# Optimization experiments

Measured on AMD Instinct MI355X. Metric: run time of the kernel, lower is better.

Reference implementation:

```python
import jax, jax.numpy as jnp
import numpy as np

B, TM1, K, H = 256, 127, 128, 256  # batch, time_step-1, input_size, hidden

def setup_inputs() -> dict:
    key = jax.random.key(0)
    ks = jax.random.split(key, 7)
    s_ih = 1.0 / np.sqrt(H)
    return {
        "input_data": jax.random.normal(ks[0], (B, TM1, K), dtype=jnp.float32),
        "W_ih": jax.random.uniform(ks[1], (4 * H, K), jnp.float32, -s_ih, s_ih),
        "W_hh": jax.random.uniform(ks[2], (4 * H, H), jnp.float32, -s_ih, s_ih),
        "b_ih": jax.random.uniform(ks[3], (4 * H,), jnp.float32, -s_ih, s_ih),
        "b_hh": jax.random.uniform(ks[4], (4 * H,), jnp.float32, -s_ih, s_ih),
        "fc_w": jax.random.uniform(ks[5], (1, 2 * H + TM1), jnp.float32, -s_ih, s_ih),
        "fc_b": jax.random.uniform(ks[6], (1,), jnp.float32, -s_ih, s_ih),
    }

def reference(input_data, W_ih, W_hh, b_ih, b_hh, fc_w, fc_b):
    b, tm1, k = input_data.shape
    h_dim = W_hh.shape[1]
    w = fc_w[0]
    W_h, W_c, W_x = w[:h_dim], w[h_dim:2 * h_dim], w[2 * h_dim:]
    # attention score contribution from each series' full history: constant over steps
    x_score = jnp.einsum('btk,t->bk', input_data, W_x) + fc_b[0]  # (B, K)
    bias = b_ih + b_hh

    def step(carry, xt):
        h, c = carry  # (B, H) each; xt: (B, K) values at current timestep
        scores = x_score + (h @ W_h + c @ W_c)[:, None]  # (B, K)
        alpha = jax.nn.softmax(scores, axis=-1)
        x = alpha * xt  # attention-weighted input
        gates = x @ W_ih.T + h @ W_hh.T + bias  # (B, 4H), torch gate order i,f,g,o
        i, f, g, o = jnp.split(gates, 4, axis=-1)
        c_new = jax.nn.sigmoid(f) * c + jax.nn.sigmoid(i) * jnp.tanh(g)
        h_new = jax.nn.sigmoid(o) * jnp.tanh(c_new)
        return (h_new, c_new), (x, h_new)

    h0 = jnp.zeros((b, h_dim), input_data.dtype)
    c0 = jnp.zeros((b, h_dim), input_data.dtype)
    xt_seq = jnp.swapaxes(input_data, 0, 1)  # (TM1, B, K)
    _, (xs, hs) = jax.lax.scan(step, (h0, c0), xt_seq)
    weight = jnp.swapaxes(xs, 0, 1)        # (B, TM1, K)
    encode_weight = jnp.swapaxes(hs, 0, 1)  # (B, TM1, H)
    return weight, encode_weight
```

## Files before the change

kernel.cpp:

```cpp
#include <hip/hip_runtime.h>
#include <hip/hip_bf16.h>
#include <stdint.h>

#define Bn 256
#define Tn 127
#define Kn 128
#define Hn 256

typedef float f32x4 __attribute__((ext_vector_type(4)));
typedef short s16x8 __attribute__((ext_vector_type(8)));

#define GX_BYTES   66584576ULL
#define REC_OFF    66584576ULL
#define REC_BYTES  1048576ULL

__device__ __forceinline__ float bf2f(unsigned short b){
  union { unsigned u; float f; } v; v.u = ((unsigned)b) << 16; return v.f;
}
__device__ __forceinline__ unsigned short f2bf_rn(float f){
  union { __hip_bfloat16 h; unsigned short s; } u;
  u.h = __float2bfloat16(f);
  return u.s;
}
__device__ __forceinline__ s16x8 cvt8(f32x4 a, f32x4 b){
  union { __hip_bfloat162 h2; unsigned short s[2]; } u0,u1,u2,u3;
  u0.h2 = __float22bfloat162_rn(float2{a[0],a[1]});
  u1.h2 = __float22bfloat162_rn(float2{a[2],a[3]});
  u2.h2 = __float22bfloat162_rn(float2{b[0],b[1]});
  u3.h2 = __float22bfloat162_rn(float2{b[2],b[3]});
  s16x8 r;
  r[0]=(short)u0.s[0]; r[1]=(short)u0.s[1]; r[2]=(short)u1.s[0]; r[3]=(short)u1.s[1];
  r[4]=(short)u2.s[0]; r[5]=(short)u2.s[1]; r[6]=(short)u3.s[0]; r[7]=(short)u3.s[1];
  return r;
}
__device__ __forceinline__ float sigf(float x){ return 1.f/(1.f+__expf(-x)); }
__device__ __forceinline__ float tanh_fast(float x){
  float ax = fabsf(x);
  float e = __expf(-2.f*ax);
  float t = (1.f - e)/(1.f + e);
  return x < 0.f ? -t : t;
}

__global__ __launch_bounds__(256) void phase0_kernel(
    const float* __restrict__ in, const float* __restrict__ fc_w,
    float* __restrict__ out)
{
  const int b    = blockIdx.x;
  const int tid  = threadIdx.x;
  const int k    = tid & 127;
  const int half = tid >> 7;
  __shared__ float wx[Tn+1];
  __shared__ float partial[2][128];
  __shared__ float red[8];
  __shared__ float alpha_s[128];
  if (tid < Tn) wx[tid] = fc_w[2*Hn + tid];
  __syncthreads();

  const float* ib = in + (size_t)b*Tn*Kn;
  const int t0 = half*64, t1 = half ? Tn : 64;
  float acc = 0.f;
  for (int t=t0; t<t1; t++) acc += ib[t*Kn + k] * wx[t];
  partial[half][k] = acc;
  __syncthreads();
  const float tot = partial[0][k] + partial[1][k];

  float mx = tot;
#pragma unroll
  for (int o=32;o>0;o>>=1) mx = fmaxf(mx, __shfl_xor(mx, o));
  const int wv = tid >> 6;
  if ((tid & 63) == 0) red[wv] = mx;
  __syncthreads();
  mx = fmaxf(fmaxf(red[0],red[1]), fmaxf(red[2],red[3]));
  float e = __expf(tot - mx);
  float sm = e;
#pragma unroll
  for (int o=32;o>0;o>>=1) sm += __shfl_xor(sm, o);
  if ((tid & 63) == 0) red[4+wv] = sm;
  __syncthreads();
  if (half == 0) alpha_s[k] = e / (red[4] + red[5]);
  __syncthreads();

  const int k4 = tid & 31;
  const int tr = tid >> 5;
  const f32x4 al4 = *(const f32x4*)&alpha_s[k4*4];
  float* ob = out + (size_t)b*Tn*Kn;
  for (int t=tr; t<Tn; t+=8){
    f32x4 v = *(const f32x4*)(ib + t*Kn + k4*4);
    v[0]*=al4[0]; v[1]*=al4[1]; v[2]*=al4[2]; v[3]*=al4[3];
    *(f32x4*)(ob + t*Kn + k4*4) = v;
  }
}

__global__ __launch_bounds__(256) void gx_kernel(
    const float* __restrict__ xw, const float* __restrict__ W_ih,
    const float* __restrict__ b_ih, const float* __restrict__ b_hh,
    __hip_bfloat16* __restrict__ gx)
{
  const int g    = blockIdx.x & 31;
  const int tpb  = blockIdx.x >> 5;
  const int tid  = threadIdx.x;
  const int wv   = tid >> 6;
  const int lane = tid & 63;
  const int c    = lane & 15;
  const int quad = lane >> 4;

  const int b  = g*8 + (c & 7);

  s16x8 afr[4][4];
#pragma unroll
  for (int tpi=0; tpi<4; tpi++){
    const int t0 = (tpb*4 + tpi)*2;
    const int tt = min(t0 + (c >> 3), Tn-1);
    const float* xp = xw + ((size_t)b*Tn + tt)*Kn + quad*8;
#pragma unroll
    for (int kb=0; kb<4; kb++)
      afr[tpi][kb] = cvt8(*(const f32x4*)(xp + kb*32), *(const f32x4*)(xp + kb*32 + 4));
  }

  const int tof = (quad >> 1);
  const int mh  = (quad & 1) * 4;

  for (int j = wv*16; j < wv*16+16; j++){
    const int n = j*16 + c;
    const float bias = b_ih[n] + b_hh[n];
    const float* wp = W_ih + (size_t)n*Kn + quad*8;
    s16x8 bfr[4];
#pragma unroll
    for (int kb=0; kb<4; kb++)
      bfr[kb] = cvt8(*(const f32x4*)(wp + kb*32), *(const f32x4*)(wp + kb*32 + 4));
    const int G = j >> 4, rem = j & 15, s = rem >> 3, w8 = rem & 7;
#pragma unroll
    for (int tpi=0; tpi<4; tpi++){
      f32x4 acc = {bias, bias, bias, bias};
#pragma unroll
      for (int kb=0; kb<4; kb++)
        acc = __builtin_amdgcn_mfma_f32_16x16x32_bf16(afr[tpi][kb], bfr[kb], acc, 0,0,0);
      const int trow = (tpb*4 + tpi)*2 + tof;
      if (trow < Tn){
        __hip_bfloat16* dst = gx +
          (((((size_t)g*Tn + trow)*2 + s)*8 + w8)*4 + G)*128 + c*8 + mh;
        ushort4 pk;
        pk.x = f2bf_rn(acc[0]); pk.y = f2bf_rn(acc[1]);
        pk.z = f2bf_rn(acc[2]); pk.w = f2bf_rn(acc[3]);
        *(ushort4*)dst = pk;
      }
    }
  }
}

__global__ __launch_bounds__(512, 2) void scan_kernel(
    const float* __restrict__ W_hh, float* __restrict__ out,
    const __hip_bfloat16* __restrict__ gx,
    unsigned long long* __restrict__ rec)
{
  const int bid  = blockIdx.x;
  const int s    = (bid >> 3) & 1;
  const int g    = (bid & 7) | ((bid >> 4) << 3);
  const int b0   = g * 8;
  const int tid  = threadIdx.x;
  const int w    = tid >> 6;
  const int lane = tid & 63;
  const int c    = lane & 15;
  const int quad = lane >> 4;
  const int u    = s*128 + w*16 + c;

  __shared__ __align__(16) unsigned short hhi[2*8*272];
  __shared__ __align__(16) unsigned short hlo[2*8*272];

  s16x8 whh[4][8];
#pragma unroll
  for (int G=0; G<4; G++){
    const float* p0 = W_hh + (size_t)(G*Hn + u)*Hn + quad*8;
#pragma unroll
    for (int kb=0; kb<8; kb++)
      whh[G][kb] = cvt8(*(const f32x4*)(p0 + kb*32), *(const f32x4*)(p0 + kb*32 + 4));
  }

  const int rsel0 = (quad >> 1) * 2;
  const int prr0  = rsel0 ^ 2;
  const int m0    = (quad & 1)*4 + rsel0;
  float cst[2] = {0.f, 0.f};

  const size_t enc_base = (size_t)Bn*Tn*Kn;
  unsigned long long* rec_mine  = rec + ((size_t)g*2 + s)*2048;
  unsigned long long* rec_other = rec + ((size_t)g*2 + (1-s))*2048;

  const int rq   = lane >> 4;
  const int r_m0 = (rq & 1)*4 + (rq >> 1)*2;
  const int r_u  = w*16 + c;
  const int rk   = (1-s)*128 + r_u;

  const __hip_bfloat16* gxg = gx + ((((size_t)g*Tn)*2 + s)*8 + w)*4*128;

  ushort4 gxr[4];
  if (quad < 2){
    const __hip_bfloat16* gp0 = gxg + c*8 + quad*4;
#pragma unroll
    for (int G=0; G<4; G++) gxr[G] = *(const ushort4*)(gp0 + G*128);
  }

  for (int t=0; t<Tn; t++){
    const int buf  = (t & 1) * 8*272;
    const int nbuf = ((t+1) & 1) * 8*272;

    f32x4 acc[4];
#pragma unroll
    for (int G=0; G<4; G++){
      if (quad < 2){
        acc[G][0]=bf2f(gxr[G].x); acc[G][1]=bf2f(gxr[G].y);
        acc[G][2]=bf2f(gxr[G].z); acc[G][3]=bf2f(gxr[G].w);
      } else {
        acc[G][0]=0.f; acc[G][1]=0.f; acc[G][2]=0.f; acc[G][3]=0.f;
      }
    }

    if (t > 0){
      const unsigned short* hb = (c < 8) ? &hhi[buf + c*272] : &hlo[buf + (c-8)*272];
#pragma unroll
      for (int kb=0; kb<8; kb++){
        const s16x8 af = *(const s16x8*)(hb + kb*32 + quad*8);
        acc[0] = __builtin_amdgcn_mfma_f32_16x16x32_bf16(af, whh[0][kb], acc[0],0,0,0);
        acc[1] = __builtin_amdgcn_mfma_f32_16x16x32_bf16(af, whh[1][kb], acc[1],0,0,0);
        acc[2] = __builtin_amdgcn_mfma_f32_16x16x32_bf16(af, whh[2][kb], acc[2],0,0,0);
        acc[3] = __builtin_amdgcn_mfma_f32_16x16x32_bf16(af, whh[3][kb], acc[3],0,0,0);
      }
    }

    float hv[2];
#pragma unroll
    for (int rp=0; rp<2; rp++){
      const int rr  = rsel0 + rp;
      const int prr = prr0 + rp;
      const float gi = acc[0][rr] + __shfl_xor(acc[0][prr], 32);
      const float gf = acc[1][rr] + __shfl_xor(acc[1][prr], 32);
      const float gg = acc[2][rr] + __shfl_xor(acc[2][prr], 32);
      const float go = acc[3][rr] + __shfl_xor(acc[3][prr], 32);
      const float cn = sigf(gf)*cst[rp] + sigf(gi)*tanh_fast(gg);
      cst[rp] = cn;
      hv[rp] = sigf(go)*tanh_fast(cn);
    }

    unsigned short hi[2], lo[2];
    hi[0] = f2bf_rn(hv[0]); lo[0] = f2bf_rn(hv[0] - bf2f(hi[0]));
    hi[1] = f2bf_rn(hv[1]); lo[1] = f2bf_rn(hv[1] - bf2f(hi[1]));
    if (t < Tn-1){
      const unsigned tg16 = ((unsigned)(t+1)) << 16;
      const unsigned long long w0 =
          (unsigned long long)((unsigned)hi[0] | tg16) |
          ((unsigned long long)((unsigned)hi[1] | tg16) << 32);
      const unsigned long long w1 =
          (unsigned long long)((unsigned)lo[0] | tg16) |
          ((unsigned long long)((unsigned)lo[1] | tg16) << 32);
      unsigned long long* rm = rec_mine + (size_t)(t & 1)*1024 + 2*tid;
      __hip_atomic_store(rm,   w0, __ATOMIC_RELAXED, __HIP_MEMORY_SCOPE_AGENT);
      __hip_atomic_store(rm+1, w1, __ATOMIC_RELAXED, __HIP_MEMORY_SCOPE_AGENT);
    }

#pragma unroll
    for (int rp=0; rp<2; rp++){
      const int m = m0 + rp;
      hhi[nbuf + m*272 + u] = hi[rp];
      hlo[nbuf + m*272 + u] = lo[rp];
      out[enc_base + ((size_t)(b0+m)*Tn + t)*Hn + u] = hv[rp];
    }

    if (t+1 < Tn && quad < 2){
      const __hip_bfloat16* gp = gxg + (size_t)(t+1)*2*8*4*128 + c*8 + quad*4;
#pragma unroll
      for (int G=0; G<4; G++) gxr[G] = *(const ushort4*)(gp + G*128);
    }

    if (t < Tn-1){
      const unsigned long long tg = (unsigned long long)(t+1);
      const unsigned long long* ro = rec_other + (size_t)(t & 1)*1024 + 2*tid;
      unsigned long long w0, w1;
      for (;;){
        w0 = __hip_atomic_load(ro,   __ATOMIC_RELAXED, __HIP_MEMORY_SCOPE_AGENT);
        w1 = __hip_atomic_load(ro+1, __ATOMIC_RELAXED, __HIP_MEMORY_SCOPE_AGENT);
        if ( ((w0 >> 16) & 0xffffu) == tg && (w0 >> 48) == tg &&
             ((w1 >> 16) & 0xffffu) == tg && (w1 >> 48) == tg ) break;
        __builtin_amdgcn_s_sleep(1);
      }
      hhi[nbuf + r_m0*272 + rk]     = (unsigned short)(w0 & 0xffffu);
      hlo[nbuf + r_m0*272 + rk]     = (unsigned short)(w1 & 0xffffu);
      hhi[nbuf + (r_m0+1)*272 + rk] = (unsigned short)((w0 >> 32) & 0xffffu);
      hlo[nbuf + (r_m0+1)*272 + rk] = (unsigned short)((w1 >> 32) & 0xffffu);
    }

    __syncthreads();
  }
}

extern "C" void kernel_launch(void* const* d_in, const int* in_sizes, int n_in,
                              void* d_out, int out_size, void* d_ws, size_t ws_size,
                              hipStream_t stream) {
  const float* input = (const float*)d_in[0];
  const float* W_ih  = (const float*)d_in[1];
  const float* W_hh  = (const float*)d_in[2];
  const float* b_ih  = (const float*)d_in[3];
  const float* b_hh  = (const float*)d_in[4];
  const float* fc_w  = (const float*)d_in[5];
  float* out = (float*)d_out;

  char* wsb = (char*)d_ws;
  __hip_bfloat16* gxp = (__hip_bfloat16*)wsb;
  unsigned long long* rec = (unsigned long long*)(wsb + REC_OFF);

  hipMemsetAsync(rec, 0, REC_BYTES, stream);
  phase0_kernel<<<Bn, 256, 0, stream>>>(input, fc_w, out);
  gx_kernel<<<512, 256, 0, stream>>>(out, W_ih, b_ih, b_hh, gxp);
  scan_kernel<<<64, 512, 0, stream>>>(W_hh, out, gxp, rec);
}
```

Before: 474.7 us.

## Add L2-local fast path for cross-block hidden-state exchange with fallback

The scan kernel's per-step exchange of hidden-state halves between paired blocks gets a second record buffer. Each step writes a 128-bit store through the plain path and also does the existing agent-scope atomic stores. The consumer polls with sc0 128-bit loads for a bounded number of spins before falling back to the old atomic polling loop. This aims to cut the latency of the inter-block handshake on the serial critical path. The fast path assumes both blocks see the same L2, which may not hold on MI355X's multi-XCD layout, so it relies on the miss counter to switch itself off, and it adds extra stores every step.

```diff
diff --git a/kernel.cpp b/kernel.cpp
--- a/kernel.cpp
+++ b/kernel.cpp
@@ -9,10 +9,12 @@
 
 typedef float f32x4 __attribute__((ext_vector_type(4)));
 typedef short s16x8 __attribute__((ext_vector_type(8)));
-
-#define GX_BYTES   66584576ULL
-#define REC_OFF    66584576ULL
-#define REC_BYTES  1048576ULL
+typedef unsigned int u32x4 __attribute__((ext_vector_type(4)));
+
+#define GX_BYTES    66584576ULL
+#define RECL2_OFF   66584576ULL
+#define REC_BYTES   1048576ULL
+#define RECIC_OFF   (RECL2_OFF + REC_BYTES)
 
 __device__ __forceinline__ float bf2f(unsigned short b){
   union { unsigned u; float f; } v; v.u = ((unsigned)b) << 16; return v.f;
@@ -39,6 +41,16 @@
   float e = __expf(-2.f*ax);
   float t = (1.f - e)/(1.f + e);
   return x < 0.f ? -t : t;
+}
+
+__device__ __forceinline__ u32x4 ld_b128_sc0(const void* p){
+  u32x4 r;
+  asm volatile("global_load_dwordx4 %0, %1, off sc0\n\ts_waitcnt vmcnt(0)"
+               : "=v"(r) : "v"(p) : "memory");
+  return r;
+}
+__device__ __forceinline__ void st_b128_l2(void* p, u32x4 v){
+  asm volatile("global_store_dwordx4 %0, %1, off" :: "v"(p), "v"(v) : "memory");
 }
 
 __global__ __launch_bounds__(256) void phase0_kernel(
@@ -151,7 +163,7 @@
 __global__ __launch_bounds__(512, 2) void scan_kernel(
     const float* __restrict__ W_hh, float* __restrict__ out,
     const __hip_bfloat16* __restrict__ gx,
-    unsigned long long* __restrict__ rec)
+    unsigned long long* __restrict__ recL2, unsigned long long* __restrict__ recIC)
 {
   const int bid  = blockIdx.x;
   const int s    = (bid >> 3) & 1;
@@ -182,8 +194,10 @@
   float cst[2] = {0.f, 0.f};
 
   const size_t enc_base = (size_t)Bn*Tn*Kn;
-  unsigned long long* rec_mine  = rec + ((size_t)g*2 + s)*2048;
-  unsigned long long* rec_other = rec + ((size_t)g*2 + (1-s))*2048;
+  unsigned long long* recL2_mine  = recL2 + ((size_t)g*2 + s)*2048;
+  unsigned long long* recL2_other = recL2 + ((size_t)g*2 + (1-s))*2048;
+  unsigned long long* recIC_mine  = recIC + ((size_t)g*2 + s)*2048;
+  unsigned long long* recIC_other = recIC + ((size_t)g*2 + (1-s))*2048;
 
   const int rq   = lane >> 4;
   const int r_m0 = (rq & 1)*4 + (rq >> 1)*2;
@@ -198,6 +212,9 @@
 #pragma unroll
     for (int G=0; G<4; G++) gxr[G] = *(const ushort4*)(gp0 + G*128);
   }
+
+  bool fastok = true;
+  int  misses = 0;
 
   for (int t=0; t<Tn; t++){
     const int buf  = (t & 1) * 8*272;
@@ -245,15 +262,17 @@
     hi[1] = f2bf_rn(hv[1]); lo[1] = f2bf_rn(hv[1] - bf2f(hi[1]));
     if (t < Tn-1){
       const unsigned tg16 = ((unsigned)(t+1)) << 16;
+      u32x4 r;
+      r[0] = (unsigned)hi[0] | tg16; r[1] = (unsigned)hi[1] | tg16;
+      r[2] = (unsigned)lo[0] | tg16; r[3] = (unsigned)lo[1] | tg16;
+      st_b128_l2(recL2_mine + (size_t)(t & 1)*1024 + 2*tid, r);
       const unsigned long long w0 =
-          (unsigned long long)((unsigned)hi[0] | tg16) |
-          ((unsigned long long)((unsigned)hi[1] | tg16) << 32);
+          (unsigned long long)r[0] | ((unsigned long long)r[1] << 32);
       const unsigned long long w1 =
-          (unsigned long long)((unsigned)lo[0] | tg16) |
-          ((unsigned long long)((unsigned)lo[1] | tg16) << 32);
-      unsigned long long* rm = rec_mine + (size_t)(t & 1)*1024 + 2*tid;
-      __hip_atomic_store(rm,   w0, __ATOMIC_RELAXED, __HIP_MEMORY_SCOPE_AGENT);
-      __hip_atomic_store(rm+1, w1, __ATOMIC_RELAXED, __HIP_MEMORY_SCOPE_AGENT);
+          (unsigned long long)r[2] | ((unsigned long long)r[3] << 32);
+      unsigned long long* rmIC = recIC_mine + (size_t)(t & 1)*1024 + 2*tid;
+      __hip_atomic_store(rmIC,   w0, __ATOMIC_RELAXED, __HIP_MEMORY_SCOPE_AGENT);
+      __hip_atomic_store(rmIC+1, w1, __ATOMIC_RELAXED, __HIP_MEMORY_SCOPE_AGENT);
     }
 
 #pragma unroll
@@ -271,20 +290,43 @@
     }
 
     if (t < Tn-1){
-      const unsigned long long tg = (unsigned long long)(t+1);
-      const unsigned long long* ro = rec_other + (size_t)(t & 1)*1024 + 2*tid;
-      unsigned long long w0, w1;
-      for (;;){
-        w0 = __hip_atomic_load(ro,   __ATOMIC_RELAXED, __HIP_MEMORY_SCOPE_AGENT);
-        w1 = __hip_atomic_load(ro+1, __ATOMIC_RELAXED, __HIP_MEMORY_SCOPE_AGENT);
-        if ( ((w0 >> 16) & 0xffffu) == tg && (w0 >> 48) == tg &&
-             ((w1 >> 16) & 0xffffu) == tg && (w1 >> 48) == tg ) break;
-        __builtin_amdgcn_s_sleep(1);
-      }
-      hhi[nbuf + r_m0*272 + rk]     = (unsigned short)(w0 & 0xffffu);
-      hlo[nbuf + r_m0*272 + rk]     = (unsigned short)(w1 & 0xffffu);
-      hhi[nbuf + (r_m0+1)*272 + rk] = (unsigned short)((w0 >> 32) & 0xffffu);
-      hlo[nbuf + (r_m0+1)*272 + rk] = (unsigned short)((w1 >> 32) & 0xffffu);
+      const unsigned tg = (unsigned)(t+1);
+      const unsigned long long* roL2 = recL2_other + (size_t)(t & 1)*1024 + 2*tid;
+      const unsigned long long* roIC = recIC_other + (size_t)(t & 1)*1024 + 2*tid;
+      unsigned short vh0, vh1, vl0, vl1;
+      bool got = false;
+      if (fastok){
+        const int nspin = (t == 0) ? 4000 : 64;
+        for (int sp=0; sp<nspin; ++sp){
+          u32x4 r = ld_b128_sc0(roL2);
+          if ((r[0]>>16)==tg && (r[1]>>16)==tg && (r[2]>>16)==tg && (r[3]>>16)==tg){
+            vh0=(unsigned short)r[0]; vh1=(unsigned short)r[1];
+            vl0=(unsigned short)r[2]; vl1=(unsigned short)r[3];
+            got = true; break;
+          }
+        }
+        if (!got){ if (++misses >= 2) fastok = false; }
+        else misses = 0;
+      }
+      if (!got){
+        for (;;){
+          const unsigned long long w0 =
+            __hip_atomic_load(roIC,   __ATOMIC_RELAXED, __HIP_MEMORY_SCOPE_AGENT);
+          const unsigned long long w1 =
+            __hip_atomic_load(roIC+1, __ATOMIC_RELAXED, __HIP_MEMORY_SCOPE_AGENT);
+          if (((w0 >> 16) & 0xffffu) == tg && (w0 >> 48) == tg &&
+              ((w1 >> 16) & 0xffffu) == tg && (w1 >> 48) == tg){
+            vh0=(unsigned short)w0; vh1=(unsigned short)(w0 >> 32);
+            vl0=(unsigned short)w1; vl1=(unsigned short)(w1 >> 32);
+            break;
+          }
+          __builtin_amdgcn_s_sleep(1);
+        }
+      }
+      hhi[nbuf + r_m0*272 + rk]     = vh0;
+      hhi[nbuf + (r_m0+1)*272 + rk] = vh1;
+      hlo[nbuf + r_m0*272 + rk]     = vl0;
+      hlo[nbuf + (r_m0+1)*272 + rk] = vl1;
     }
 
     __syncthreads();
@@ -304,10 +346,12 @@
 
   char* wsb = (char*)d_ws;
   __hip_bfloat16* gxp = (__hip_bfloat16*)wsb;
-  unsigned long long* rec = (unsigned long long*)(wsb + REC_OFF);
-
-  hipMemsetAsync(rec, 0, REC_BYTES, stream);
+  unsigned long long* recL2 = (unsigned long long*)(wsb + RECL2_OFF);
+  const bool dual = (ws_size >= RECIC_OFF + REC_BYTES);
+  unsigned long long* recIC = dual ? (unsigned long long*)(wsb + RECIC_OFF) : recL2;
+
+  hipMemsetAsync(recL2, 0, dual ? 2*REC_BYTES : REC_BYTES, stream);
   phase0_kernel<<<Bn, 256, 0, stream>>>(input, fc_w, out);
   gx_kernel<<<512, 256, 0, stream>>>(out, W_ih, b_ih, b_hh, gxp);
-  scan_kernel<<<64, 512, 0, stream>>>(W_hh, out, gxp, rec);
-}
+  scan_kernel<<<64, 512, 0, stream>>>(W_hh, out, gxp, recL2, recIC);
+}
```

After: 1.496 ms. 3.15x slower.

## Split recurrent matmul over K across block pairs with partial-sum exchange

Applied to the files above, without the earlier changes.

Adds a scan variant in which the two blocks serving a batch group each own half of the hidden input dimension. Each block computes its own partial gate sums plus the partial sums for the other block's units, and swaps those through tagged 64-bit atomic stores in global memory with spin-wait polling, instead of exchanging full hidden states. The weights are converted to bf16 once by a new kernel, so the gx and scan kernels load them directly instead of converting per thread. The new path only runs when the workspace is large enough. Packing a step tag into the low mantissa bits drops some precision from the partial sums, and the per-step cross-block handshake now sits on the critical path.

```diff
diff --git a/kernel.cpp b/kernel.cpp
--- a/kernel.cpp
+++ b/kernel.cpp
@@ -11,8 +11,12 @@
 typedef short s16x8 __attribute__((ext_vector_type(8)));
 
 #define GX_BYTES   66584576ULL
-#define REC_OFF    66584576ULL
+#define PART_OFF   66584576ULL
+#define PART_BYTES 2097152ULL
 #define REC_BYTES  1048576ULL
+#define WIH_OFF    (PART_OFF + PART_BYTES)
+#define WHH_OFF    (WIH_OFF + 262144ULL)
+#define WS_NEED    (WHH_OFF + 524288ULL)
 
 __device__ __forceinline__ float bf2f(unsigned short b){
   union { unsigned u; float f; } v; v.u = ((unsigned)b) << 16; return v.f;
@@ -39,6 +43,20 @@
   float e = __expf(-2.f*ax);
   float t = (1.f - e)/(1.f + e);
   return x < 0.f ? -t : t;
+}
+
+__global__ __launch_bounds__(256) void wconv_kernel(
+    const float* __restrict__ Wih, const float* __restrict__ Whh,
+    __hip_bfloat16* __restrict__ Bih, __hip_bfloat16* __restrict__ Bhh)
+{
+  const int i = blockIdx.x*256 + threadIdx.x;
+  const float* src; __hip_bfloat16* dst; int j;
+  if (i < 16384){ src = Wih; dst = Bih; j = i; }
+  else          { src = Whh; dst = Bhh; j = i - 16384; }
+  const f32x4 a = *(const f32x4*)(src + (size_t)j*8);
+  const f32x4 b = *(const f32x4*)(src + (size_t)j*8 + 4);
+  s16x8 r = cvt8(a, b);
+  *(s16x8*)(dst + (size_t)j*8) = r;
 }
 
 __global__ __launch_bounds__(256) void phase0_kernel(
@@ -93,8 +111,9 @@
 
 __global__ __launch_bounds__(256) void gx_kernel(
     const float* __restrict__ xw, const float* __restrict__ W_ih,
+    const __hip_bfloat16* __restrict__ Bih,
     const float* __restrict__ b_ih, const float* __restrict__ b_hh,
-    __hip_bfloat16* __restrict__ gx)
+    __hip_bfloat16* __restrict__ gx, int pre)
 {
   const int g    = blockIdx.x & 31;
   const int tpb  = blockIdx.x >> 5;
@@ -123,11 +142,17 @@
   for (int j = wv*16; j < wv*16+16; j++){
     const int n = j*16 + c;
     const float bias = b_ih[n] + b_hh[n];
-    const float* wp = W_ih + (size_t)n*Kn + quad*8;
     s16x8 bfr[4];
-#pragma unroll
-    for (int kb=0; kb<4; kb++)
-      bfr[kb] = cvt8(*(const f32x4*)(wp + kb*32), *(const f32x4*)(wp + kb*32 + 4));
+    if (pre){
+      const __hip_bfloat16* wp = Bih + (size_t)n*Kn + quad*8;
+#pragma unroll
+      for (int kb=0; kb<4; kb++) bfr[kb] = *(const s16x8*)(wp + kb*32);
+    } else {
+      const float* wp = W_ih + (size_t)n*Kn + quad*8;
+#pragma unroll
+      for (int kb=0; kb<4; kb++)
+        bfr[kb] = cvt8(*(const f32x4*)(wp + kb*32), *(const f32x4*)(wp + kb*32 + 4));
+    }
     const int G = j >> 4, rem = j & 15, s = rem >> 3, w8 = rem & 7;
 #pragma unroll
     for (int tpi=0; tpi<4; tpi++){
@@ -148,7 +173,175 @@
   }
 }
 
-__global__ __launch_bounds__(512, 2) void scan_kernel(
+__global__ __launch_bounds__(512, 2) void scan_ksplit(
+    const __hip_bfloat16* __restrict__ Bhh,
+    float* __restrict__ out, const __hip_bfloat16* __restrict__ gx,
+    unsigned long long* __restrict__ part)
+{
+  const int bid  = blockIdx.x;
+  const int s    = (bid >> 3) & 1;
+  const int g    = (bid & 7) | ((bid >> 4) << 3);
+  const int b0   = g * 8;
+  const int tid  = threadIdx.x;
+  const int w    = tid >> 6;
+  const int lane = tid & 63;
+  const int c    = lane & 15;
+  const int quad = lane >> 4;
+  const int ul   = w*16 + c;
+  const int u    = s*128 + ul;
+
+  __shared__ __align__(16) unsigned short hhi[2*8*136];
+  __shared__ __align__(16) unsigned short hlo[2*8*136];
+
+  s16x8 whO[4][4], whT[4][4];
+#pragma unroll
+  for (int G=0; G<4; G++){
+    const __hip_bfloat16* pO = Bhh + ((size_t)(G*256 + s*128     + ul))*256 + s*128 + quad*8;
+    const __hip_bfloat16* pT = Bhh + ((size_t)(G*256 + (1-s)*128 + ul))*256 + s*128 + quad*8;
+#pragma unroll
+    for (int kb=0; kb<4; kb++){
+      whO[G][kb] = *(const s16x8*)(pO + kb*32);
+      whT[G][kb] = *(const s16x8*)(pT + kb*32);
+    }
+  }
+
+  const int rsel0 = (quad >> 1) * 2;
+  const int prr0  = rsel0 ^ 2;
+  const int m0    = (quad & 1)*4 + rsel0;
+  float cst[2] = {0.f, 0.f};
+
+  const size_t enc_base = (size_t)Bn*Tn*Kn;
+  unsigned long long* pmine  = part + (((size_t)g*2 + s)*2)*2048 + (size_t)tid*4;
+  unsigned long long* pother = part + (((size_t)g*2 + (1-s))*2)*2048 + (size_t)tid*4;
+
+  const __hip_bfloat16* gxg = gx + ((((size_t)g*Tn)*2 + s)*8 + w)*4*128;
+
+  ushort4 gxr[4];
+  if (quad < 2){
+    const __hip_bfloat16* gp0 = gxg + c*8 + quad*4;
+#pragma unroll
+    for (int G=0; G<4; G++) gxr[G] = *(const ushort4*)(gp0 + G*128);
+  }
+
+  for (int t=0; t<Tn; t++){
+    const int buf  = (t & 1) * 8*136;
+    const int nbuf = ((t+1) & 1) * 8*136;
+
+    f32x4 accO[4];
+#pragma unroll
+    for (int G=0; G<4; G++){
+      if (quad < 2){
+        accO[G][0]=bf2f(gxr[G].x); accO[G][1]=bf2f(gxr[G].y);
+        accO[G][2]=bf2f(gxr[G].z); accO[G][3]=bf2f(gxr[G].w);
+      } else {
+        accO[G][0]=0.f; accO[G][1]=0.f; accO[G][2]=0.f; accO[G][3]=0.f;
+      }
+    }
+
+    if (t > 0){
+      const unsigned short* hb = (c < 8) ? &hhi[buf + c*136] : &hlo[buf + (c-8)*136];
+      s16x8 af[4];
+#pragma unroll
+      for (int kb=0; kb<4; kb++)
+        af[kb] = *(const s16x8*)(hb + kb*32 + quad*8);
+
+      f32x4 accT[4];
+#pragma unroll
+      for (int G=0; G<4; G++){ accT[G][0]=0.f; accT[G][1]=0.f; accT[G][2]=0.f; accT[G][3]=0.f; }
+#pragma unroll
+      for (int kb=0; kb<4; kb++){
+        accT[0] = __builtin_amdgcn_mfma_f32_16x16x32_bf16(af[kb], whT[0][kb], accT[0],0,0,0);
+        accT[1] = __builtin_amdgcn_mfma_f32_16x16x32_bf16(af[kb], whT[1][kb], accT[1],0,0,0);
+        accT[2] = __builtin_amdgcn_mfma_f32_16x16x32_bf16(af[kb], whT[2][kb], accT[2],0,0,0);
+        accT[3] = __builtin_amdgcn_mfma_f32_16x16x32_bf16(af[kb], whT[3][kb], accT[3],0,0,0);
+      }
+
+      const unsigned tg = (unsigned)t & 0x7Fu;
+      unsigned long long* pm = pmine + (size_t)(t & 1)*2048;
+#pragma unroll
+      for (int G=0; G<4; G++){
+        const float p0 = accT[G][rsel0]   + __shfl_xor(accT[G][prr0],   32);
+        const float p1 = accT[G][rsel0+1] + __shfl_xor(accT[G][prr0+1], 32);
+        const unsigned d0 = (__float_as_uint(p0) & 0xFFFFFF80u) | tg;
+        const unsigned d1 = (__float_as_uint(p1) & 0xFFFFFF80u) | tg;
+        const unsigned long long q =
+            (unsigned long long)d0 | ((unsigned long long)d1 << 32);
+        __hip_atomic_store(pm + G, q, __ATOMIC_RELAXED, __HIP_MEMORY_SCOPE_AGENT);
+      }
+
+#pragma unroll
+      for (int kb=0; kb<4; kb++){
+        accO[0] = __builtin_amdgcn_mfma_f32_16x16x32_bf16(af[kb], whO[0][kb], accO[0],0,0,0);
+        accO[1] = __builtin_amdgcn_mfma_f32_16x16x32_bf16(af[kb], whO[1][kb], accO[1],0,0,0);
+        accO[2] = __builtin_amdgcn_mfma_f32_16x16x32_bf16(af[kb], whO[2][kb], accO[2],0,0,0);
+        accO[3] = __builtin_amdgcn_mfma_f32_16x16x32_bf16(af[kb], whO[3][kb], accO[3],0,0,0);
+      }
+    }
+
+    if (t+1 < Tn && quad < 2){
+      const __hip_bfloat16* gp = gxg + (size_t)(t+1)*2*8*4*128 + c*8 + quad*4;
+#pragma unroll
+      for (int G=0; G<4; G++) gxr[G] = *(const ushort4*)(gp + G*128);
+    }
+
+    float rv[4][2];
+    if (t > 0){
+      const unsigned tg = (unsigned)t & 0x7Fu;
+      const unsigned long long* po = pother + (size_t)(t & 1)*2048;
+      unsigned long long q0,q1,q2,q3;
+      for (;;){
+        q0 = __hip_atomic_load(po+0, __ATOMIC_RELAXED, __HIP_MEMORY_SCOPE_AGENT);
+        q1 = __hip_atomic_load(po+1, __ATOMIC_RELAXED, __HIP_MEMORY_SCOPE_AGENT);
+        q2 = __hip_atomic_load(po+2, __ATOMIC_RELAXED, __HIP_MEMORY_SCOPE_AGENT);
+        q3 = __hip_atomic_load(po+3, __ATOMIC_RELAXED, __HIP_MEMORY_SCOPE_AGENT);
+        if ( ((unsigned)q0 & 0x7Fu)==tg && ((unsigned)(q0>>32) & 0x7Fu)==tg &&
+             ((unsigned)q1 & 0x7Fu)==tg && ((unsigned)(q1>>32) & 0x7Fu)==tg &&
+             ((unsigned)q2 & 0x7Fu)==tg && ((unsigned)(q2>>32) & 0x7Fu)==tg &&
+             ((unsigned)q3 & 0x7Fu)==tg && ((unsigned)(q3>>32) & 0x7Fu)==tg ) break;
+        __builtin_amdgcn_s_sleep(1);
+      }
+      rv[0][0] = __uint_as_float((unsigned)q0 & 0xFFFFFF80u);
+      rv[0][1] = __uint_as_float((unsigned)(q0>>32) & 0xFFFFFF80u);
+      rv[1][0] = __uint_as_float((unsigned)q1 & 0xFFFFFF80u);
+      rv[1][1] = __uint_as_float((unsigned)(q1>>32) & 0xFFFFFF80u);
+      rv[2][0] = __uint_as_float((unsigned)q2 & 0xFFFFFF80u);
+      rv[2][1] = __uint_as_float((unsigned)(q2>>32) & 0xFFFFFF80u);
+      rv[3][0] = __uint_as_float((unsigned)q3 & 0xFFFFFF80u);
+      rv[3][1] = __uint_as_float((unsigned)(q3>>32) & 0xFFFFFF80u);
+    } else {
+#pragma unroll
+      for (int G=0; G<4; G++){ rv[G][0]=0.f; rv[G][1]=0.f; }
+    }
+
+    float hv[2];
+#pragma unroll
+    for (int rp=0; rp<2; rp++){
+      const int rr  = rsel0 + rp;
+      const int prr = prr0 + rp;
+      const float gi = accO[0][rr] + __shfl_xor(accO[0][prr], 32) + rv[0][rp];
+      const float gf = accO[1][rr] + __shfl_xor(accO[1][prr], 32) + rv[1][rp];
+      const float gg = accO[2][rr] + __shfl_xor(accO[2][prr], 32) + rv[2][rp];
+      const float go = accO[3][rr] + __shfl_xor(accO[3][prr], 32) + rv[3][rp];
+      const float cn = sigf(gf)*cst[rp] + sigf(gi)*tanh_fast(gg);
+      cst[rp] = cn;
+      hv[rp] = sigf(go)*tanh_fast(cn);
+    }
+
+#pragma unroll
+    for (int rp=0; rp<2; rp++){
+      const unsigned short hi = f2bf_rn(hv[rp]);
+      const unsigned short lo = f2bf_rn(hv[rp] - bf2f(hi));
+      const int m = m0 + rp;
+      hhi[nbuf + m*136 + ul] = hi;
+      hlo[nbuf + m*136 + ul] = lo;
+      out[enc_base + ((size_t)(b0+m)*Tn + t)*Hn + u] = hv[rp];
+    }
+
+    __syncthreads();
+  }
+}
+
+__global__ __launch_bounds__(512, 2) void scan_nsplit(
     const float* __restrict__ W_hh, float* __restrict__ out,
     const __hip_bfloat16* __restrict__ gx,
     unsigned long long* __restrict__ rec)
@@ -304,10 +497,23 @@
 
   char* wsb = (char*)d_ws;
   __hip_bfloat16* gxp = (__hip_bfloat16*)wsb;
-  unsigned long long* rec = (unsigned long long*)(wsb + REC_OFF);
-
-  hipMemsetAsync(rec, 0, REC_BYTES, stream);
-  phase0_kernel<<<Bn, 256, 0, stream>>>(input, fc_w, out);
-  gx_kernel<<<512, 256, 0, stream>>>(out, W_ih, b_ih, b_hh, gxp);
-  scan_kernel<<<64, 512, 0, stream>>>(W_hh, out, gxp, rec);
-}
+  unsigned long long* part = (unsigned long long*)(wsb + PART_OFF);
+
+  const int full = (ws_size >= WS_NEED) ? 1 : 0;
+
+  if (full){
+    __hip_bfloat16* Bih = (__hip_bfloat16*)(wsb + WIH_OFF);
+    __hip_bfloat16* Bhh = (__hip_bfloat16*)(wsb + WHH_OFF);
+    hipMemsetAsync(part, 0, PART_BYTES, stream);
+    wconv_kernel<<<192, 256, 0, stream>>>(W_ih, W_hh, Bih, Bhh);
+    phase0_kernel<<<Bn, 256, 0, stream>>>(input, fc_w, out);
+    gx_kernel<<<512, 256, 0, stream>>>(out, W_ih, Bih, b_ih, b_hh, gxp, 1);
+    scan_ksplit<<<64, 512, 0, stream>>>(Bhh, out, gxp, part);
+  } else {
+    hipMemsetAsync(part, 0, REC_BYTES, stream);
+    phase0_kernel<<<Bn, 256, 0, stream>>>(input, fc_w, out);
+    gx_kernel<<<512, 256, 0, stream>>>(out, W_ih, (const __hip_bfloat16*)W_ih,
+                                       b_ih, b_hh, gxp, 0);
+    scan_nsplit<<<64, 512, 0, stream>>>(W_hh, out, gxp, part);
+  }
+}
```

After: 604.9 us. 27.4% more time.

## Overlap peer h-state wait with own-half MFMA; pre-convert weights to bf16

Applied to the files above, without the earlier changes.

The scan loop now runs the MFMAs for its own half of the hidden state before polling for the partner block's half. It then fills that half into the current buffer, synchronises, and finishes the remaining MFMAs, so the cross-block wait overlaps with compute. The spin loop also drops its sleep. A separate kernel pre-converts W_ih and W_hh to bf16 in the workspace so gx_kernel and scan_kernel load bf16 directly instead of converting fp32 in each block. This adds an extra __syncthreads per step and a small extra launch, and the busy-wait without sleep may increase memory polling pressure.

```diff
diff --git a/kernel.cpp b/kernel.cpp
--- a/kernel.cpp
+++ b/kernel.cpp
@@ -13,6 +13,9 @@
 #define GX_BYTES   66584576ULL
 #define REC_OFF    66584576ULL
 #define REC_BYTES  1048576ULL
+#define WIH_OFF    (REC_OFF + REC_BYTES)
+#define WHH_OFF    (WIH_OFF + 262144ULL)
+#define WS_NEED    (WHH_OFF + 524288ULL)
 
 __device__ __forceinline__ float bf2f(unsigned short b){
   union { unsigned u; float f; } v; v.u = ((unsigned)b) << 16; return v.f;
@@ -39,6 +42,20 @@
   float e = __expf(-2.f*ax);
   float t = (1.f - e)/(1.f + e);
   return x < 0.f ? -t : t;
+}
+
+__global__ __launch_bounds__(256) void wconv_kernel(
+    const float* __restrict__ Wih, const float* __restrict__ Whh,
+    __hip_bfloat16* __restrict__ Bih, __hip_bfloat16* __restrict__ Bhh)
+{
+  const int i = blockIdx.x*256 + threadIdx.x;
+  const float* src; __hip_bfloat16* dst; int j;
+  if (i < 16384){ src = Wih; dst = Bih; j = i; }
+  else          { src = Whh; dst = Bhh; j = i - 16384; }
+  const f32x4 a = *(const f32x4*)(src + (size_t)j*8);
+  const f32x4 b = *(const f32x4*)(src + (size_t)j*8 + 4);
+  s16x8 r = cvt8(a, b);
+  *(s16x8*)(dst + (size_t)j*8) = r;
 }
 
 __global__ __launch_bounds__(256) void phase0_kernel(
@@ -93,8 +110,9 @@
 
 __global__ __launch_bounds__(256) void gx_kernel(
     const float* __restrict__ xw, const float* __restrict__ W_ih,
+    const __hip_bfloat16* __restrict__ Bih,
     const float* __restrict__ b_ih, const float* __restrict__ b_hh,
-    __hip_bfloat16* __restrict__ gx)
+    __hip_bfloat16* __restrict__ gx, int pre)
 {
   const int g    = blockIdx.x & 31;
   const int tpb  = blockIdx.x >> 5;
@@ -123,11 +141,17 @@
   for (int j = wv*16; j < wv*16+16; j++){
     const int n = j*16 + c;
     const float bias = b_ih[n] + b_hh[n];
-    const float* wp = W_ih + (size_t)n*Kn + quad*8;
     s16x8 bfr[4];
-#pragma unroll
-    for (int kb=0; kb<4; kb++)
-      bfr[kb] = cvt8(*(const f32x4*)(wp + kb*32), *(const f32x4*)(wp + kb*32 + 4));
+    if (pre){
+      const __hip_bfloat16* wp = Bih + (size_t)n*Kn + quad*8;
+#pragma unroll
+      for (int kb=0; kb<4; kb++) bfr[kb] = *(const s16x8*)(wp + kb*32);
+    } else {
+      const float* wp = W_ih + (size_t)n*Kn + quad*8;
+#pragma unroll
+      for (int kb=0; kb<4; kb++)
+        bfr[kb] = cvt8(*(const f32x4*)(wp + kb*32), *(const f32x4*)(wp + kb*32 + 4));
+    }
     const int G = j >> 4, rem = j & 15, s = rem >> 3, w8 = rem & 7;
 #pragma unroll
     for (int tpi=0; tpi<4; tpi++){
@@ -149,9 +173,9 @@
 }
 
 __global__ __launch_bounds__(512, 2) void scan_kernel(
-    const float* __restrict__ W_hh, float* __restrict__ out,
-    const __hip_bfloat16* __restrict__ gx,
-    unsigned long long* __restrict__ rec)
+    const float* __restrict__ W_hh, const __hip_bfloat16* __restrict__ Bhh,
+    float* __restrict__ out, const __hip_bfloat16* __restrict__ gx,
+    unsigned long long* __restrict__ rec, int pre)
 {
   const int bid  = blockIdx.x;
   const int s    = (bid >> 3) & 1;
@@ -168,13 +192,25 @@
   __shared__ __align__(16) unsigned short hlo[2*8*272];
 
   s16x8 whh[4][8];
-#pragma unroll
-  for (int G=0; G<4; G++){
-    const float* p0 = W_hh + (size_t)(G*Hn + u)*Hn + quad*8;
-#pragma unroll
-    for (int kb=0; kb<8; kb++)
-      whh[G][kb] = cvt8(*(const f32x4*)(p0 + kb*32), *(const f32x4*)(p0 + kb*32 + 4));
-  }
+  if (pre){
+#pragma unroll
+    for (int G=0; G<4; G++){
+      const __hip_bfloat16* p0 = Bhh + (size_t)(G*Hn + u)*Hn + quad*8;
+#pragma unroll
+      for (int kb=0; kb<8; kb++) whh[G][kb] = *(const s16x8*)(p0 + kb*32);
+    }
+  } else {
+#pragma unroll
+    for (int G=0; G<4; G++){
+      const float* p0 = W_hh + (size_t)(G*Hn + u)*Hn + quad*8;
+#pragma unroll
+      for (int kb=0; kb<8; kb++)
+        whh[G][kb] = cvt8(*(const f32x4*)(p0 + kb*32), *(const f32x4*)(p0 + kb*32 + 4));
+    }
+  }
+
+  const int kO = s*4;
+  const int kT = (1-s)*4;
 
   const int rsel0 = (quad >> 1) * 2;
   const int prr0  = rsel0 ^ 2;
@@ -216,8 +252,37 @@
 
     if (t > 0){
       const unsigned short* hb = (c < 8) ? &hhi[buf + c*272] : &hlo[buf + (c-8)*272];
-#pragma unroll
-      for (int kb=0; kb<8; kb++){
+
+#pragma unroll
+      for (int k4i=0; k4i<4; k4i++){
+        const int kb = kO + k4i;
+        const s16x8 af = *(const s16x8*)(hb + kb*32 + quad*8);
+        acc[0] = __builtin_amdgcn_mfma_f32_16x16x32_bf16(af, whh[0][kb], acc[0],0,0,0);
+        acc[1] = __builtin_amdgcn_mfma_f32_16x16x32_bf16(af, whh[1][kb], acc[1],0,0,0);
+        acc[2] = __builtin_amdgcn_mfma_f32_16x16x32_bf16(af, whh[2][kb], acc[2],0,0,0);
+        acc[3] = __builtin_amdgcn_mfma_f32_16x16x32_bf16(af, whh[3][kb], acc[3],0,0,0);
+      }
+
+      {
+        const unsigned long long tg = (unsigned long long)t;
+        const unsigned long long* ro = rec_other + (size_t)((t-1) & 1)*1024 + 2*tid;
+        unsigned long long w0, w1;
+        for (;;){
+          w0 = __hip_atomic_load(ro,   __ATOMIC_RELAXED, __HIP_MEMORY_SCOPE_AGENT);
+          w1 = __hip_atomic_load(ro+1, __ATOMIC_RELAXED, __HIP_MEMORY_SCOPE_AGENT);
+          if ( ((w0 >> 16) & 0xffffu) == tg && (w0 >> 48) == tg &&
+               ((w1 >> 16) & 0xffffu) == tg && (w1 >> 48) == tg ) break;
+        }
+        hhi[buf + r_m0*272 + rk]     = (unsigned short)(w0 & 0xffffu);
+        hlo[buf + r_m0*272 + rk]     = (unsigned short)(w1 & 0xffffu);
+        hhi[buf + (r_m0+1)*272 + rk] = (unsigned short)((w0 >> 32) & 0xffffu);
+        hlo[buf + (r_m0+1)*272 + rk] = (unsigned short)((w1 >> 32) & 0xffffu);
+      }
+      __syncthreads();
+
+#pragma unroll
+      for (int k4i=0; k4i<4; k4i++){
+        const int kb = kT + k4i;
         const s16x8 af = *(const s16x8*)(hb + kb*32 + quad*8);
         acc[0] = __builtin_amdgcn_mfma_f32_16x16x32_bf16(af, whh[0][kb], acc[0],0,0,0);
         acc[1] = __builtin_amdgcn_mfma_f32_16x16x32_bf16(af, whh[1][kb], acc[1],0,0,0);
@@ -270,23 +335,6 @@
       for (int G=0; G<4; G++) gxr[G] = *(const ushort4*)(gp + G*128);
     }
 
-    if (t < Tn-1){
-      const unsigned long long tg = (unsigned long long)(t+1);
-      const unsigned long long* ro = rec_other + (size_t)(t & 1)*1024 + 2*tid;
-      unsigned long long w0, w1;
-      for (;;){
-        w0 = __hip_atomic_load(ro,   __ATOMIC_RELAXED, __HIP_MEMORY_SCOPE_AGENT);
-        w1 = __hip_atomic_load(ro+1, __ATOMIC_RELAXED, __HIP_MEMORY_SCOPE_AGENT);
-        if ( ((w0 >> 16) & 0xffffu) == tg && (w0 >> 48) == tg &&
-             ((w1 >> 16) & 0xffffu) == tg && (w1 >> 48) == tg ) break;
-        __builtin_amdgcn_s_sleep(1);
-      }
-      hhi[nbuf + r_m0*272 + rk]     = (unsigned short)(w0 & 0xffffu);
-      hlo[nbuf + r_m0*272 + rk]     = (unsigned short)(w1 & 0xffffu);
-      hhi[nbuf + (r_m0+1)*272 + rk] = (unsigned short)((w0 >> 32) & 0xffffu);
-      hlo[nbuf + (r_m0+1)*272 + rk] = (unsigned short)((w1 >> 32) & 0xffffu);
-    }
-
     __syncthreads();
   }
 }
@@ -306,8 +354,14 @@
   __hip_bfloat16* gxp = (__hip_bfloat16*)wsb;
   unsigned long long* rec = (unsigned long long*)(wsb + REC_OFF);
 
+  const int full = (ws_size >= WS_NEED) ? 1 : 0;
+  __hip_bfloat16* Bih = full ? (__hip_bfloat16*)(wsb + WIH_OFF) : (__hip_bfloat16*)W_ih;
+  __hip_bfloat16* Bhh = full ? (__hip_bfloat16*)(wsb + WHH_OFF) : (__hip_bfloat16*)W_hh;
+
   hipMemsetAsync(rec, 0, REC_BYTES, stream);
+  if (full)
+    wconv_kernel<<<192, 256, 0, stream>>>(W_ih, W_hh, Bih, Bhh);
   phase0_kernel<<<Bn, 256, 0, stream>>>(input, fc_w, out);
-  gx_kernel<<<512, 256, 0, stream>>>(out, W_ih, b_ih, b_hh, gxp);
-  scan_kernel<<<64, 512, 0, stream>>>(W_hh, out, gxp, rec);
-}
+  gx_kernel<<<512, 256, 0, stream>>>(out, W_ih, Bih, b_ih, b_hh, gxp, full);
+  scan_kernel<<<64, 512, 0, stream>>>(W_hh, Bhh, out, gxp, rec, full);
+}
```

New measurement: 1.251 ms. 2.64x slower.
